# Kernel tuning notes

Hardware: AMD Instinct MI355X
Metric: run time of the kernel (lower is better)

The kernel has to match this reference:

```python
import jax, jax.numpy as jnp
import numpy as np

B, L, D = 2, 2048, 768
H = 12
HD = D // H  # 64
SCALE = HD ** -0.5


def setup_inputs() -> dict:
    key = jax.random.key(0)
    k1, k2, k3 = jax.random.split(key, 3)
    x = jax.random.normal(k1, (B, L, D), dtype=jnp.float32)
    mask = jnp.ones((B, L), dtype=jnp.int32)
    # nn.Linear weights: [out_features, in_features]
    Wqkv = jax.random.normal(k2, (3 * D, D), dtype=jnp.float32) * (D ** -0.5)
    bqkv = jnp.zeros((3 * D,), dtype=jnp.float32)
    Wout = jax.random.normal(k3, (D, D), dtype=jnp.float32) * (D ** -0.5)
    bout = jnp.zeros((D,), dtype=jnp.float32)
    return {"x": x, "mask": mask, "Wqkv": Wqkv, "bqkv": bqkv, "Wout": Wout, "bout": bout}


def reference(x, mask, Wqkv, bqkv, Wout, bout):
    Bx, Lx, Dx = x.shape
    # qkv projection: [B,L,3D] -> [3,B,H,L,HD]
    qkv = x @ Wqkv.T + bqkv
    qkv = qkv.reshape(Bx, Lx, 3, H, HD).transpose(2, 0, 3, 1, 4)
    q, k, v = qkv[0], qkv[1], qkv[2]
    # scores [B,H,L,L]
    attn = jnp.einsum('bhqd,bhkd->bhqk', q, k) * SCALE
    attn = jnp.where(mask[:, None, None, :] == 0, -jnp.inf, attn)
    attn = jax.nn.softmax(attn, axis=-1)
    # dropout p=0.0 -> identity
    out = jnp.einsum('bhqk,bhkd->bhqd', attn, v)
    out = out.transpose(0, 2, 1, 3).reshape(Bx, Lx, Dx)
    return out @ Wout.T + bout
```

## Files before the change

### kernel.cpp

```cpp
#include <hip/hip_runtime.h>
#include <hip/hip_bf16.h>

#define DEV __device__ __forceinline__

typedef __bf16 bf16_t;
typedef bf16_t bf16x8 __attribute__((ext_vector_type(8)));
typedef float f32x4 __attribute__((ext_vector_type(4)));
typedef float f32x16 __attribute__((ext_vector_type(16)));
typedef unsigned int u32x4 __attribute__((ext_vector_type(4)));

constexpr int Bc = 2, Lc = 2048, Dc = 768, Hc = 12, HDc = 64;
constexpr int NTOK = Bc * Lc;
constexpr int QKVN = 3 * Dc;
constexpr float ATT_SCALE = 0.125f;
constexpr float LOG2E = 1.44269504088896f;

DEV unsigned short f2bf(float f) {
  unsigned int u = __builtin_bit_cast(unsigned int, f);
  u += 0x7FFFu + ((u >> 16) & 1u);
  return (unsigned short)(u >> 16);
}

DEV bf16x8 ld16(const unsigned short* p) {
  return __builtin_bit_cast(bf16x8, *reinterpret_cast<const u32x4*>(p));
}

DEV unsigned cvtpk(float lo, float hi) {
  unsigned r;
  asm("v_cvt_pk_bf16_f32 %0, %1, %2" : "=v"(r) : "v"(lo), "v"(hi));
  return r;
}

DEV void gload16(const unsigned short* g, unsigned short* l) {
  __builtin_amdgcn_global_load_lds(
      (const __attribute__((address_space(1))) unsigned int*)g,
      (__attribute__((address_space(3))) unsigned int*)l, 16, 0, 0);
}

__global__ __launch_bounds__(256) void prep_kernel(
    const float* __restrict__ x, const float* __restrict__ Wqkv,
    const float* __restrict__ Wout, const int* __restrict__ mask,
    unsigned short* __restrict__ xb, unsigned short* __restrict__ wqkvb,
    unsigned short* __restrict__ woutb, float* __restrict__ mb,
    int* __restrict__ mflag) {
  const int bid = blockIdx.x, tid = threadIdx.x;
  const float* src; unsigned short* dst; int base;
  if (bid < 3072)      { src = x;    dst = xb;    base = bid; }
  else if (bid < 4800) { src = Wqkv; dst = wqkvb; base = bid - 3072; }
  else if (bid < 5376) { src = Wout; dst = woutb; base = bid - 4800; }
  else {
    int i = (bid - 5376) * 256 + tid;
    int mv = mask[i];
    mb[i] = mv ? 0.f : -1e30f;
    unsigned long long anyz = __ballot(mv == 0);
    if ((tid & 63) == 0) mflag[i >> 6] = (anyz != 0ull) ? 1 : 0;
    return;
  }
  int i = (base * 256 + tid) * 4;
  float4 v = *reinterpret_cast<const float4*>(src + i);
  ushort4 o;
  o.x = f2bf(v.x); o.y = f2bf(v.y); o.z = f2bf(v.z); o.w = f2bf(v.w);
  *reinterpret_cast<ushort4*>(dst + i) = o;
}

template <int MODE>
__global__ __launch_bounds__(256) void gemm_bt(
    const unsigned short* __restrict__ A,
    const unsigned short* __restrict__ Bw,
    const float* __restrict__ bias,
    unsigned short* __restrict__ qb, unsigned short* __restrict__ kb,
    unsigned short* __restrict__ vtb,
    float* __restrict__ Y,
    int M, int N, int K) {
  constexpr int BM = (MODE == 0) ? 128 : 64;
  constexpr int BN = 96, BK = 64;
  constexpr int AI = BM * BK / 2048;
  constexpr int MR = BM / 32;
  __shared__ alignas(16) unsigned short a_lds[BM * BK];
  __shared__ alignas(16) unsigned short b_lds[BN * BK];
  __shared__ alignas(16) unsigned short qk_patch[(MODE == 0) ? 4 : 1][16][56];

  const int tid = threadIdx.x;
  const int lane = tid & 63;
  const int l15 = lane & 15, lg = lane >> 4;
  const int wave = tid >> 6;
  const int wr = wave >> 1, wc = wave & 1;

  const int nm = M / BM;
  const int nwg = nm * (N / BN);
  const int t = (blockIdx.x & 7) * (nwg >> 3) + (blockIdx.x >> 3);
  const int m0 = (t % nm) * BM;
  const int n0 = (t / nm) * BN;

  f32x4 acc[MR][3] = {};

  for (int k0 = 0; k0 < K; k0 += BK) {
#pragma unroll
    for (int i = 0; i < AI; ++i) {
      int cc = i * 256 + tid;
      int row = cc >> 3, col = (cc & 7) * 8;
      gload16(A + (size_t)(m0 + row) * K + k0 + col, &a_lds[(i * 256 + wave * 64) * 8]);
    }
#pragma unroll
    for (int i = 0; i < 3; ++i) {
      int cc = i * 256 + tid;
      int row = cc >> 3, col = (cc & 7) * 8;
      gload16(Bw + (size_t)(n0 + row) * K + k0 + col, &b_lds[(i * 256 + wave * 64) * 8]);
    }
    __syncthreads();
#pragma unroll
    for (int kk = 0; kk < 2; ++kk) {
      bf16x8 af[MR], bfr[3];
#pragma unroll
      for (int m = 0; m < MR; ++m) {
        int row = wr * (MR * 16) + m * 16 + l15;
        af[m] = ld16(&a_lds[row * BK + kk * 32 + lg * 8]);
      }
#pragma unroll
      for (int n = 0; n < 3; ++n) {
        int row = wc * 48 + n * 16 + l15;
        bfr[n] = ld16(&b_lds[row * BK + kk * 32 + lg * 8]);
      }
#pragma unroll
      for (int m = 0; m < MR; ++m)
#pragma unroll
        for (int n = 0; n < 3; ++n)
          acc[m][n] = __builtin_amdgcn_mfma_f32_16x16x32_bf16(af[m], bfr[n], acc[m][n], 0, 0, 0);
    }
    __syncthreads();
  }

  if constexpr (MODE == 0) {
    const int base_col = n0 + wc * 48;
    const int s = n0 / Dc;
    if (s == 2) {
#pragma unroll
      for (int m = 0; m < 4; ++m) {
        int lq = m0 + wr * 64 + m * 16 + lg * 4;
        int b = lq >> 11, lql = lq & 2047;
#pragma unroll
        for (int n = 0; n < 3; ++n) {
          int cbase = base_col + n * 16;
          int h = (cbase % Dc) >> 6;
          int d = (cbase & 63) + l15;
          float bv = bias[cbase + l15];
          ushort4 o;
#pragma unroll
          for (int j = 0; j < 4; ++j)
            ((unsigned short*)&o)[j] = f2bf(acc[m][n][j] + bv);
          *reinterpret_cast<ushort4*>(
              vtb + ((size_t)(b * Hc + h) * HDc + d) * Lc + lql) = o;
        }
      }
    } else {
      unsigned short* dst = (s == 0) ? qb : kb;
      const float sc = (s == 0) ? (ATT_SCALE * LOG2E) : 1.0f;
#pragma unroll
      for (int m = 0; m < 4; ++m) {
#pragma unroll
        for (int n = 0; n < 3; ++n) {
          float bv = bias[base_col + n * 16 + l15];
#pragma unroll
          for (int j = 0; j < 4; ++j)
            qk_patch[wave][lg * 4 + j][n * 16 + l15] =
                f2bf((acc[m][n][j] + bv) * sc);
        }
#pragma unroll
        for (int i = 0; i < 2; ++i) {
          int task = i * 64 + lane;
          if (task < 96) {
            int r = task / 6, ch = task - r * 6;
            int gcol = base_col + ch * 8;
            int h = (gcol % Dc) >> 6;
            int d0 = gcol & 63;
            int lq = m0 + wr * 64 + m * 16 + r;
            int b = lq >> 11, lql = lq & 2047;
            u32x4 v = *reinterpret_cast<const u32x4*>(&qk_patch[wave][r][ch * 8]);
            *reinterpret_cast<u32x4*>(
                dst + ((size_t)(b * Hc + h) * Lc + lql) * HDc + d0) = v;
          }
        }
      }
    }
  } else {
#pragma unroll
    for (int m = 0; m < MR; ++m) {
      int row_base = m0 + wr * (MR * 16) + m * 16 + lg * 4;
#pragma unroll
      for (int n = 0; n < 3; ++n) {
        int col = n0 + wc * 48 + n * 16 + l15;
        float bv = bias[col];
#pragma unroll
        for (int j = 0; j < 4; ++j)
          Y[(size_t)(row_base + j) * Dc + col] = acc[m][n][j] + bv;
      }
    }
  }
}

__global__ __launch_bounds__(256) void attn_kernel(
    const unsigned short* __restrict__ qb,
    const unsigned short* __restrict__ kb,
    const unsigned short* __restrict__ vtb,
    const float* __restrict__ mb,
    const int* __restrict__ mflag,
    unsigned short* __restrict__ aout) {
  __shared__ alignas(16) unsigned short k_lds[4][4096];
  __shared__ alignas(16) unsigned short v_lds[2][4096];
  __shared__ float l_lds[2][32];
  const int tid = threadIdx.x;
  const int lane = tid & 63;
  const int l31 = lane & 31;
  const int hi = lane >> 5;
  const int wave = tid >> 6;
  const int ws = wave & 1;
  const int g = wave >> 1;
  const int f = blockIdx.x;
  const int loc = f >> 3;
  const int bh = (f & 7) * 3 + (loc >> 5);
  const int b = bh / Hc, h = bh % Hc;
  const int q0 = (loc & 31) * 64 + ws * 32;

  const unsigned short* Kbh = kb + (size_t)bh * Lc * HDc;
  const unsigned short* Vbh = vtb + (size_t)bh * HDc * Lc;
  const float* mbb = mb + b * Lc + hi * 4;
  const int* mfp = mflag + b * (Lc / 64);

  unsigned long long mbits;
  {
    int mv = (lane < 32) ? mfp[lane] : 0;
    mbits = __ballot(mv != 0);
  }

  bf16x8 qf[4];
  {
    const unsigned short* Qp = qb + ((size_t)bh * Lc + q0 + l31) * HDc + hi * 8;
#pragma unroll
    for (int c = 0; c < 4; ++c) qf[c] = ld16(Qp + c * 16);
  }

  bf16x8 onesf;
  {
    u32x4 ow = {0x3F803F80u, 0x3F803F80u, 0x3F803F80u, 0x3F803F80u};
    onesf = __builtin_bit_cast(bf16x8, ow);
  }

  f32x16 accO[2] = {};
  f32x16 accL = {};

  const int j0 = wave * 2, j1 = j0 + 1;
  const int r80 = j0 * 8 + (lane >> 3), r81 = r80 + 8;
  const int csw0 = (((lane & 7) ^ (lane >> 3) ^ (j0 & 3))) << 3;
  const int csw1 = (((lane & 7) ^ (lane >> 3) ^ (j1 & 3))) << 3;
  const unsigned short* kp0 = Kbh + (size_t)r80 * HDc + csw0;
  const unsigned short* kp1 = Kbh + (size_t)r81 * HDc + csw1;
  const unsigned short* vp0 = Vbh + (size_t)r80 * Lc + csw0;
  const unsigned short* vp1 = Vbh + (size_t)r81 * Lc + csw1;

#define STAGEK(buf)                               \
  {                                               \
    gload16(kp0, &k_lds[buf][j0 * 512]);          \
    gload16(kp1, &k_lds[buf][j1 * 512]);          \
    kp0 += 64 * HDc; kp1 += 64 * HDc;             \
  }
#define STAGEV(buf)                               \
  {                                               \
    gload16(vp0, &v_lds[buf][j0 * 512]);          \
    gload16(vp1, &v_lds[buf][j1 * 512]);          \
    vp0 += 64; vp1 += 64;                         \
  }

  const int swz = ((l31 & 7) ^ (l31 >> 3)) << 3;
  const int krow = (g * 32 + l31) * 64;

  STAGEK(0) STAGEK(1) STAGEV(0)
  asm volatile("s_waitcnt vmcnt(0)" ::: "memory");
  __builtin_amdgcn_s_barrier();
  f32x16 s = {};
#pragma unroll
  for (int c = 0; c < 4; ++c) {
    int ch = (((c * 2 + hi) << 3) ^ swz);
    s = __builtin_amdgcn_mfma_f32_32x32x16_bf16(
        ld16(&k_lds[0][0] + krow + ch), qf[c], s, 0, 0, 0);
  }
  STAGEK(2) STAGEV(1)

  constexpr int NSTEP = Lc / 64;
  for (int t = 0; t < NSTEP; ++t) {
    if (t + 3 < NSTEP) STAGEK((t + 3) & 3)

    f32x16 s2 = {};
    if (t + 1 < NSTEP) {
      const unsigned short* kl = &k_lds[(t + 1) & 3][0];
      __builtin_amdgcn_s_setprio(1);
#pragma unroll
      for (int c = 0; c < 4; ++c) {
        int ch = (((c * 2 + hi) << 3) ^ swz);
        s2 = __builtin_amdgcn_mfma_f32_32x32x16_bf16(
            ld16(kl + krow + ch), qf[c], s2, 0, 0, 0);
      }
      __builtin_amdgcn_s_setprio(0);
    }

    if ((mbits >> t) & 1ull) {
      const int kvt = t * 64 + g * 32;
#pragma unroll
      for (int gg = 0; gg < 4; ++gg) {
        float4 m0v = *reinterpret_cast<const float4*>(mbb + kvt + gg * 8);
        s[gg * 4 + 0] += m0v.x; s[gg * 4 + 1] += m0v.y;
        s[gg * 4 + 2] += m0v.z; s[gg * 4 + 3] += m0v.w;
      }
    }
#pragma unroll
    for (int i = 0; i < 16; ++i) s[i] = __builtin_amdgcn_exp2f(s[i]);
    bf16x8 pf[2];
#pragma unroll
    for (int c = 0; c < 2; ++c) {
      const int o = c * 8;
      unsigned pk01 = cvtpk(s[o + 0], s[o + 1]);
      unsigned pk23 = cvtpk(s[o + 2], s[o + 3]);
      unsigned pk45 = cvtpk(s[o + 4], s[o + 5]);
      unsigned pk67 = cvtpk(s[o + 6], s[o + 7]);
      asm("v_permlane32_swap_b32 %0, %1" : "+v"(pk01), "+v"(pk45));
      asm("v_permlane32_swap_b32 %0, %1" : "+v"(pk23), "+v"(pk67));
      u32x4 w = {pk01, pk23, pk45, pk67};
      pf[c] = __builtin_bit_cast(bf16x8, w);
    }
    accL = __builtin_amdgcn_mfma_f32_32x32x16_bf16(onesf, pf[0], accL, 0, 0, 0);
    accL = __builtin_amdgcn_mfma_f32_32x32x16_bf16(onesf, pf[1], accL, 0, 0, 0);
    {
      const unsigned short* vl = &v_lds[t & 1][0];
      __builtin_amdgcn_s_setprio(1);
#pragma unroll
      for (int dt = 0; dt < 2; ++dt) {
#pragma unroll
        for (int c = 0; c < 2; ++c) {
          int ch = (((g * 4 + c * 2 + hi) << 3) ^ swz);
          accO[dt] = __builtin_amdgcn_mfma_f32_32x32x16_bf16(
              ld16(vl + (dt * 32 + l31) * 64 + ch), pf[c], accO[dt], 0, 0, 0);
        }
      }
      __builtin_amdgcn_s_setprio(0);
    }
    if (t < NSTEP - 3) {
      asm volatile("s_waitcnt vmcnt(2)" ::: "memory");
    } else {
      asm volatile("s_waitcnt vmcnt(0)" ::: "memory");
    }
    __builtin_amdgcn_s_barrier();
    __builtin_amdgcn_sched_barrier(0);
    if (t + 2 < NSTEP) STAGEV((t) & 1)
    s = s2;
  }

  __syncthreads();
  const float l_run = accL[0];
  float* mO = (float*)&k_lds[0][0];
  if (g == 1) {
#pragma unroll
    for (int dt = 0; dt < 2; ++dt)
#pragma unroll
      for (int i = 0; i < 16; ++i)
        mO[(ws * 32 + dt * 16 + i) * 64 + lane] = accO[dt][i];
    if (hi == 0) l_lds[ws][l31] = l_run;
  }
  __syncthreads();
  if (g == 0) {
    float rl = 1.0f / (l_run + l_lds[ws][l31]);
    const int q = q0 + l31;
    unsigned short* op = aout + ((size_t)(b * Lc + q)) * Dc + h * HDc;
#pragma unroll
    for (int dt = 0; dt < 2; ++dt)
#pragma unroll
      for (int gg = 0; gg < 4; ++gg) {
        ushort4 o;
#pragma unroll
        for (int j = 0; j < 4; ++j) {
          int i = gg * 4 + j;
          float v = (accO[dt][i] + mO[(ws * 32 + dt * 16 + i) * 64 + lane]) * rl;
          ((unsigned short*)&o)[j] = f2bf(v);
        }
        *reinterpret_cast<ushort4*>(op + dt * 32 + gg * 8 + hi * 4) = o;
      }
  }
}

extern "C" void kernel_launch(void* const* d_in, const int* in_sizes, int n_in,
                              void* d_out, int out_size, void* d_ws, size_t ws_size,
                              hipStream_t stream) {
  const float* x    = (const float*)d_in[0];
  const int*   mask = (const int*)d_in[1];
  const float* Wqkv = (const float*)d_in[2];
  const float* bqkv = (const float*)d_in[3];
  const float* Wout = (const float*)d_in[4];
  const float* bout = (const float*)d_in[5];
  float* out = (float*)d_out;

  constexpr size_t NX   = (size_t)NTOK * Dc;
  constexpr size_t NWQ  = (size_t)QKVN * Dc;
  constexpr size_t NWO  = (size_t)Dc * Dc;
  unsigned short* w = (unsigned short*)d_ws;
  unsigned short* xb    = w;            w += NX;
  unsigned short* wqkvb = w;            w += NWQ;
  unsigned short* woutb = w;            w += NWO;
  unsigned short* qbuf  = w;            w += NX;
  unsigned short* kbuf  = w;            w += NX;
  unsigned short* vtb   = w;            w += NX;
  unsigned short* aoutb = w;            w += NX;
  float* mbf = (float*)w;               w += 2 * NTOK;
  int* mflag = (int*)w;

  prep_kernel<<<5392, 256, 0, stream>>>(x, Wqkv, Wout, mask, xb, wqkvb, woutb, mbf, mflag);

  gemm_bt<0><<<(NTOK / 128) * (QKVN / 96), 256, 0, stream>>>(
      xb, wqkvb, bqkv, qbuf, kbuf, vtb, nullptr, NTOK, QKVN, Dc);

  attn_kernel<<<dim3(768), 256, 0, stream>>>(qbuf, kbuf, vtb, mbf, mflag, aoutb);

  gemm_bt<1><<<(NTOK / 64) * (Dc / 96), 256, 0, stream>>>(
      aoutb, woutb, bout, nullptr, nullptr, nullptr, out, NTOK, Dc, Dc);
}
```

Before: 93.13 us.

## Unroll attention loop by two with ping-pong scores and stagger block starts

Rewrites the KV loop as a macro unrolled by two, alternating two score registers so the s=s2 copy disappears and the loop-edge conditions become compile-time constants in the peeled tail iterations. The QK MFMA chain now starts from a constant zero accumulator. Also adds s_sleep delays at kernel start that differ by block index modulo 3, to stagger blocks so their memory and MFMA phases overlap less in lockstep. The sleeps add a small fixed latency per block and the larger unrolled body raises code size.

```diff
diff --git a/kernel.cpp b/kernel.cpp
--- a/kernel.cpp
+++ b/kernel.cpp
@@ -221,6 +221,12 @@
   const int b = bh / Hc, h = bh % Hc;
   const int q0 = (loc & 31) * 64 + ws * 32;
 
+  {
+    const int ph = f % 3;
+    if (ph == 1) { asm volatile("s_sleep 8\n\ts_sleep 8"); }
+    else if (ph == 2) { asm volatile("s_sleep 8\n\ts_sleep 8\n\ts_sleep 8\n\ts_sleep 8"); }
+  }
+
   const unsigned short* Kbh = kb + (size_t)bh * Lc * HDc;
   const unsigned short* Vbh = vtb + (size_t)bh * HDc * Lc;
   const float* mbb = mb + b * Lc + hi * 4;
@@ -247,6 +253,7 @@
 
   f32x16 accO[2] = {};
   f32x16 accL = {};
+  const f32x16 fz = {};
 
   const int j0 = wave * 2, j1 = j0 + 1;
   const int r80 = j0 * 8 + (lane >> 3), r81 = r80 + 8;
@@ -272,86 +279,90 @@
 
   const int swz = ((l31 & 7) ^ (l31 >> 3)) << 3;
   const int krow = (g * 32 + l31) * 64;
+  const int ch0 = ((0 * 2 + hi) << 3) ^ swz;
+  const int ch1 = ((1 * 2 + hi) << 3) ^ swz;
+  const int ch2 = ((2 * 2 + hi) << 3) ^ swz;
+  const int ch3 = ((3 * 2 + hi) << 3) ^ swz;
+
+#define ITER(T, SCUR, SNEXT, DOK, DOQK, VMN, DOV)                                     \
+  {                                                                                   \
+    if (DOK) STAGEK((T + 3) & 3)                                                      \
+    if (DOQK) {                                                                       \
+      const unsigned short* kl = &k_lds[(T + 1) & 3][0];                              \
+      __builtin_amdgcn_s_setprio(1);                                                  \
+      SNEXT = __builtin_amdgcn_mfma_f32_32x32x16_bf16(ld16(kl + krow + ch0), qf[0], fz, 0, 0, 0);    \
+      SNEXT = __builtin_amdgcn_mfma_f32_32x32x16_bf16(ld16(kl + krow + ch1), qf[1], SNEXT, 0, 0, 0); \
+      SNEXT = __builtin_amdgcn_mfma_f32_32x32x16_bf16(ld16(kl + krow + ch2), qf[2], SNEXT, 0, 0, 0); \
+      SNEXT = __builtin_amdgcn_mfma_f32_32x32x16_bf16(ld16(kl + krow + ch3), qf[3], SNEXT, 0, 0, 0); \
+      __builtin_amdgcn_s_setprio(0);                                                  \
+    }                                                                                 \
+    if ((mbits >> (T)) & 1ull) {                                                      \
+      const int kvt = (T) * 64 + g * 32;                                              \
+      _Pragma("unroll")                                                               \
+      for (int gg = 0; gg < 4; ++gg) {                                                \
+        float4 m0v = *reinterpret_cast<const float4*>(mbb + kvt + gg * 8);            \
+        SCUR[gg * 4 + 0] += m0v.x; SCUR[gg * 4 + 1] += m0v.y;                         \
+        SCUR[gg * 4 + 2] += m0v.z; SCUR[gg * 4 + 3] += m0v.w;                         \
+      }                                                                               \
+    }                                                                                 \
+    _Pragma("unroll")                                                                 \
+    for (int i = 0; i < 16; ++i) SCUR[i] = __builtin_amdgcn_exp2f(SCUR[i]);           \
+    bf16x8 pf[2];                                                                     \
+    _Pragma("unroll")                                                                 \
+    for (int c = 0; c < 2; ++c) {                                                     \
+      const int o = c * 8;                                                            \
+      unsigned pk01 = cvtpk(SCUR[o + 0], SCUR[o + 1]);                                \
+      unsigned pk23 = cvtpk(SCUR[o + 2], SCUR[o + 3]);                                \
+      unsigned pk45 = cvtpk(SCUR[o + 4], SCUR[o + 5]);                                \
+      unsigned pk67 = cvtpk(SCUR[o + 6], SCUR[o + 7]);                                \
+      asm("v_permlane32_swap_b32 %0, %1" : "+v"(pk01), "+v"(pk45));                   \
+      asm("v_permlane32_swap_b32 %0, %1" : "+v"(pk23), "+v"(pk67));                   \
+      u32x4 w = {pk01, pk23, pk45, pk67};                                             \
+      pf[c] = __builtin_bit_cast(bf16x8, w);                                          \
+    }                                                                                 \
+    accL = __builtin_amdgcn_mfma_f32_32x32x16_bf16(onesf, pf[0], accL, 0, 0, 0);      \
+    accL = __builtin_amdgcn_mfma_f32_32x32x16_bf16(onesf, pf[1], accL, 0, 0, 0);      \
+    {                                                                                 \
+      const unsigned short* vl = &v_lds[(T) & 1][0];                                  \
+      __builtin_amdgcn_s_setprio(1);                                                  \
+      _Pragma("unroll")                                                               \
+      for (int dt = 0; dt < 2; ++dt) {                                                \
+        _Pragma("unroll")                                                             \
+        for (int c = 0; c < 2; ++c) {                                                 \
+          int chv = (((g * 4 + c * 2 + hi) << 3) ^ swz);                              \
+          accO[dt] = __builtin_amdgcn_mfma_f32_32x32x16_bf16(                         \
+              ld16(vl + (dt * 32 + l31) * 64 + chv), pf[c], accO[dt], 0, 0, 0);       \
+        }                                                                             \
+      }                                                                               \
+      __builtin_amdgcn_s_setprio(0);                                                  \
+    }                                                                                 \
+    asm volatile("s_waitcnt vmcnt(" #VMN ")" ::: "memory");                           \
+    __builtin_amdgcn_s_barrier();                                                     \
+    __builtin_amdgcn_sched_barrier(0);                                                \
+    if (DOV) STAGEV((T) & 1)                                                          \
+  }
 
   STAGEK(0) STAGEK(1) STAGEV(0)
   asm volatile("s_waitcnt vmcnt(0)" ::: "memory");
   __builtin_amdgcn_s_barrier();
-  f32x16 s = {};
-#pragma unroll
-  for (int c = 0; c < 4; ++c) {
-    int ch = (((c * 2 + hi) << 3) ^ swz);
-    s = __builtin_amdgcn_mfma_f32_32x32x16_bf16(
-        ld16(&k_lds[0][0] + krow + ch), qf[c], s, 0, 0, 0);
+  f32x16 sA, sB;
+  {
+    const unsigned short* kl = &k_lds[0][0];
+    sA = __builtin_amdgcn_mfma_f32_32x32x16_bf16(ld16(kl + krow + ch0), qf[0], fz, 0, 0, 0);
+    sA = __builtin_amdgcn_mfma_f32_32x32x16_bf16(ld16(kl + krow + ch1), qf[1], sA, 0, 0, 0);
+    sA = __builtin_amdgcn_mfma_f32_32x32x16_bf16(ld16(kl + krow + ch2), qf[2], sA, 0, 0, 0);
+    sA = __builtin_amdgcn_mfma_f32_32x32x16_bf16(ld16(kl + krow + ch3), qf[3], sA, 0, 0, 0);
   }
   STAGEK(2) STAGEV(1)
 
-  constexpr int NSTEP = Lc / 64;
-  for (int t = 0; t < NSTEP; ++t) {
-    if (t + 3 < NSTEP) STAGEK((t + 3) & 3)
-
-    f32x16 s2 = {};
-    if (t + 1 < NSTEP) {
-      const unsigned short* kl = &k_lds[(t + 1) & 3][0];
-      __builtin_amdgcn_s_setprio(1);
-#pragma unroll
-      for (int c = 0; c < 4; ++c) {
-        int ch = (((c * 2 + hi) << 3) ^ swz);
-        s2 = __builtin_amdgcn_mfma_f32_32x32x16_bf16(
-            ld16(kl + krow + ch), qf[c], s2, 0, 0, 0);
-      }
-      __builtin_amdgcn_s_setprio(0);
-    }
-
-    if ((mbits >> t) & 1ull) {
-      const int kvt = t * 64 + g * 32;
-#pragma unroll
-      for (int gg = 0; gg < 4; ++gg) {
-        float4 m0v = *reinterpret_cast<const float4*>(mbb + kvt + gg * 8);
-        s[gg * 4 + 0] += m0v.x; s[gg * 4 + 1] += m0v.y;
-        s[gg * 4 + 2] += m0v.z; s[gg * 4 + 3] += m0v.w;
-      }
-    }
-#pragma unroll
-    for (int i = 0; i < 16; ++i) s[i] = __builtin_amdgcn_exp2f(s[i]);
-    bf16x8 pf[2];
-#pragma unroll
-    for (int c = 0; c < 2; ++c) {
-      const int o = c * 8;
-      unsigned pk01 = cvtpk(s[o + 0], s[o + 1]);
-      unsigned pk23 = cvtpk(s[o + 2], s[o + 3]);
-      unsigned pk45 = cvtpk(s[o + 4], s[o + 5]);
-      unsigned pk67 = cvtpk(s[o + 6], s[o + 7]);
-      asm("v_permlane32_swap_b32 %0, %1" : "+v"(pk01), "+v"(pk45));
-      asm("v_permlane32_swap_b32 %0, %1" : "+v"(pk23), "+v"(pk67));
-      u32x4 w = {pk01, pk23, pk45, pk67};
-      pf[c] = __builtin_bit_cast(bf16x8, w);
-    }
-    accL = __builtin_amdgcn_mfma_f32_32x32x16_bf16(onesf, pf[0], accL, 0, 0, 0);
-    accL = __builtin_amdgcn_mfma_f32_32x32x16_bf16(onesf, pf[1], accL, 0, 0, 0);
-    {
-      const unsigned short* vl = &v_lds[t & 1][0];
-      __builtin_amdgcn_s_setprio(1);
-#pragma unroll
-      for (int dt = 0; dt < 2; ++dt) {
-#pragma unroll
-        for (int c = 0; c < 2; ++c) {
-          int ch = (((g * 4 + c * 2 + hi) << 3) ^ swz);
-          accO[dt] = __builtin_amdgcn_mfma_f32_32x32x16_bf16(
-              ld16(vl + (dt * 32 + l31) * 64 + ch), pf[c], accO[dt], 0, 0, 0);
-        }
-      }
-      __builtin_amdgcn_s_setprio(0);
-    }
-    if (t < NSTEP - 3) {
-      asm volatile("s_waitcnt vmcnt(2)" ::: "memory");
-    } else {
-      asm volatile("s_waitcnt vmcnt(0)" ::: "memory");
-    }
-    __builtin_amdgcn_s_barrier();
-    __builtin_amdgcn_sched_barrier(0);
-    if (t + 2 < NSTEP) STAGEV((t) & 1)
-    s = s2;
-  }
+  for (int t = 0; t < 28; t += 2) {
+    ITER(t,     sA, sB, true, true, 2, true)
+    ITER(t + 1, sB, sA, true, true, 2, true)
+  }
+  ITER(28, sA, sB, true,  true,  2, true)
+  ITER(29, sB, sA, false, true,  0, true)
+  ITER(30, sA, sB, false, true,  0, false)
+  ITER(31, sB, sA, false, false, 0, false)
 
   __syncthreads();
   const float l_run = accL[0];
```

Measured after the change: 107.9 us. +15.8%, slower.

## Have each attention wave process two query tiles, halving block waves

Applied to the files above, without the earlier changes.

The attention block drops from four waves to two. Each wave now handles both 32-row query tiles instead of one, so every K and V fragment read from LDS feeds two MFMAs, and each wave issues four staging loads instead of two. The aim is to cut LDS read traffic per MFMA and raise per-wave instruction-level parallelism. In exchange, register pressure roughly doubles for the accumulators and score tiles, there are fewer waves to hide latency, and the wait counts are adjusted to match.

```diff
diff --git a/kernel.cpp b/kernel.cpp
--- a/kernel.cpp
+++ b/kernel.cpp
@@ -198,7 +198,7 @@
   }
 }
 
-__global__ __launch_bounds__(256) void attn_kernel(
+__global__ __launch_bounds__(128, 2) void attn_kernel(
     const unsigned short* __restrict__ qb,
     const unsigned short* __restrict__ kb,
     const unsigned short* __restrict__ vtb,
@@ -213,13 +213,12 @@
   const int l31 = lane & 31;
   const int hi = lane >> 5;
   const int wave = tid >> 6;
-  const int ws = wave & 1;
-  const int g = wave >> 1;
+  const int g = wave;
   const int f = blockIdx.x;
   const int loc = f >> 3;
   const int bh = (f & 7) * 3 + (loc >> 5);
   const int b = bh / Hc, h = bh % Hc;
-  const int q0 = (loc & 31) * 64 + ws * 32;
+  const int q0 = (loc & 31) * 64;
 
   const unsigned short* Kbh = kb + (size_t)bh * Lc * HDc;
   const unsigned short* Vbh = vtb + (size_t)bh * HDc * Lc;
@@ -232,11 +231,12 @@
     mbits = __ballot(mv != 0);
   }
 
-  bf16x8 qf[4];
-  {
-    const unsigned short* Qp = qb + ((size_t)bh * Lc + q0 + l31) * HDc + hi * 8;
-#pragma unroll
-    for (int c = 0; c < 4; ++c) qf[c] = ld16(Qp + c * 16);
+  bf16x8 qf[2][4];
+#pragma unroll
+  for (int qt = 0; qt < 2; ++qt) {
+    const unsigned short* Qp = qb + ((size_t)bh * Lc + q0 + qt * 32 + l31) * HDc + hi * 8;
+#pragma unroll
+    for (int c = 0; c < 4; ++c) qf[qt][c] = ld16(Qp + c * 16);
   }
 
   bf16x8 onesf;
@@ -245,29 +245,35 @@
     onesf = __builtin_bit_cast(bf16x8, ow);
   }
 
-  f32x16 accO[2] = {};
-  f32x16 accL = {};
-
-  const int j0 = wave * 2, j1 = j0 + 1;
-  const int r80 = j0 * 8 + (lane >> 3), r81 = r80 + 8;
-  const int csw0 = (((lane & 7) ^ (lane >> 3) ^ (j0 & 3))) << 3;
-  const int csw1 = (((lane & 7) ^ (lane >> 3) ^ (j1 & 3))) << 3;
-  const unsigned short* kp0 = Kbh + (size_t)r80 * HDc + csw0;
-  const unsigned short* kp1 = Kbh + (size_t)r81 * HDc + csw1;
-  const unsigned short* vp0 = Vbh + (size_t)r80 * Lc + csw0;
-  const unsigned short* vp1 = Vbh + (size_t)r81 * Lc + csw1;
-
-#define STAGEK(buf)                               \
-  {                                               \
-    gload16(kp0, &k_lds[buf][j0 * 512]);          \
-    gload16(kp1, &k_lds[buf][j1 * 512]);          \
-    kp0 += 64 * HDc; kp1 += 64 * HDc;             \
-  }
-#define STAGEV(buf)                               \
-  {                                               \
-    gload16(vp0, &v_lds[buf][j0 * 512]);          \
-    gload16(vp1, &v_lds[buf][j1 * 512]);          \
-    vp0 += 64; vp1 += 64;                         \
+  f32x16 accO[2][2] = {};
+  f32x16 accL[2] = {};
+
+  const unsigned short* kp[4];
+  const unsigned short* vp[4];
+#pragma unroll
+  for (int jj = 0; jj < 4; ++jj) {
+    int j = wave * 4 + jj;
+    int r8 = j * 8 + (lane >> 3);
+    int csw = (((lane & 7) ^ (lane >> 3) ^ (j & 3))) << 3;
+    kp[jj] = Kbh + (size_t)r8 * HDc + csw;
+    vp[jj] = Vbh + (size_t)r8 * Lc + csw;
+  }
+
+#define STAGEK(buf)                                                   \
+  {                                                                   \
+    _Pragma("unroll")                                                 \
+    for (int jj = 0; jj < 4; ++jj) {                                  \
+      gload16(kp[jj], &k_lds[buf][(wave * 4 + jj) * 512]);            \
+      kp[jj] += 64 * HDc;                                             \
+    }                                                                 \
+  }
+#define STAGEV(buf)                                                   \
+  {                                                                   \
+    _Pragma("unroll")                                                 \
+    for (int jj = 0; jj < 4; ++jj) {                                  \
+      gload16(vp[jj], &v_lds[buf][(wave * 4 + jj) * 512]);            \
+      vp[jj] += 64;                                                   \
+    }                                                                 \
   }
 
   const int swz = ((l31 & 7) ^ (l31 >> 3)) << 3;
@@ -276,12 +282,13 @@
   STAGEK(0) STAGEK(1) STAGEV(0)
   asm volatile("s_waitcnt vmcnt(0)" ::: "memory");
   __builtin_amdgcn_s_barrier();
-  f32x16 s = {};
+  f32x16 s[2] = {};
 #pragma unroll
   for (int c = 0; c < 4; ++c) {
     int ch = (((c * 2 + hi) << 3) ^ swz);
-    s = __builtin_amdgcn_mfma_f32_32x32x16_bf16(
-        ld16(&k_lds[0][0] + krow + ch), qf[c], s, 0, 0, 0);
+    bf16x8 kread = ld16(&k_lds[0][0] + krow + ch);
+    s[0] = __builtin_amdgcn_mfma_f32_32x32x16_bf16(kread, qf[0][c], s[0], 0, 0, 0);
+    s[1] = __builtin_amdgcn_mfma_f32_32x32x16_bf16(kread, qf[1][c], s[1], 0, 0, 0);
   }
   STAGEK(2) STAGEV(1)
 
@@ -289,15 +296,16 @@
   for (int t = 0; t < NSTEP; ++t) {
     if (t + 3 < NSTEP) STAGEK((t + 3) & 3)
 
-    f32x16 s2 = {};
+    f32x16 s2[2] = {};
     if (t + 1 < NSTEP) {
       const unsigned short* kl = &k_lds[(t + 1) & 3][0];
       __builtin_amdgcn_s_setprio(1);
 #pragma unroll
       for (int c = 0; c < 4; ++c) {
         int ch = (((c * 2 + hi) << 3) ^ swz);
-        s2 = __builtin_amdgcn_mfma_f32_32x32x16_bf16(
-            ld16(kl + krow + ch), qf[c], s2, 0, 0, 0);
+        bf16x8 kread = ld16(kl + krow + ch);
+        s2[0] = __builtin_amdgcn_mfma_f32_32x32x16_bf16(kread, qf[0][c], s2[0], 0, 0, 0);
+        s2[1] = __builtin_amdgcn_mfma_f32_32x32x16_bf16(kread, qf[1][c], s2[1], 0, 0, 0);
       }
       __builtin_amdgcn_s_setprio(0);
     }
@@ -307,27 +315,37 @@
 #pragma unroll
       for (int gg = 0; gg < 4; ++gg) {
         float4 m0v = *reinterpret_cast<const float4*>(mbb + kvt + gg * 8);
-        s[gg * 4 + 0] += m0v.x; s[gg * 4 + 1] += m0v.y;
-        s[gg * 4 + 2] += m0v.z; s[gg * 4 + 3] += m0v.w;
-      }
-    }
-#pragma unroll
-    for (int i = 0; i < 16; ++i) s[i] = __builtin_amdgcn_exp2f(s[i]);
-    bf16x8 pf[2];
-#pragma unroll
-    for (int c = 0; c < 2; ++c) {
-      const int o = c * 8;
-      unsigned pk01 = cvtpk(s[o + 0], s[o + 1]);
-      unsigned pk23 = cvtpk(s[o + 2], s[o + 3]);
-      unsigned pk45 = cvtpk(s[o + 4], s[o + 5]);
-      unsigned pk67 = cvtpk(s[o + 6], s[o + 7]);
-      asm("v_permlane32_swap_b32 %0, %1" : "+v"(pk01), "+v"(pk45));
-      asm("v_permlane32_swap_b32 %0, %1" : "+v"(pk23), "+v"(pk67));
-      u32x4 w = {pk01, pk23, pk45, pk67};
-      pf[c] = __builtin_bit_cast(bf16x8, w);
-    }
-    accL = __builtin_amdgcn_mfma_f32_32x32x16_bf16(onesf, pf[0], accL, 0, 0, 0);
-    accL = __builtin_amdgcn_mfma_f32_32x32x16_bf16(onesf, pf[1], accL, 0, 0, 0);
+#pragma unroll
+        for (int qt = 0; qt < 2; ++qt) {
+          s[qt][gg * 4 + 0] += m0v.x; s[qt][gg * 4 + 1] += m0v.y;
+          s[qt][gg * 4 + 2] += m0v.z; s[qt][gg * 4 + 3] += m0v.w;
+        }
+      }
+    }
+#pragma unroll
+    for (int qt = 0; qt < 2; ++qt)
+#pragma unroll
+      for (int i = 0; i < 16; ++i) s[qt][i] = __builtin_amdgcn_exp2f(s[qt][i]);
+    bf16x8 pf[2][2];
+#pragma unroll
+    for (int qt = 0; qt < 2; ++qt)
+#pragma unroll
+      for (int c = 0; c < 2; ++c) {
+        const int o = c * 8;
+        unsigned pk01 = cvtpk(s[qt][o + 0], s[qt][o + 1]);
+        unsigned pk23 = cvtpk(s[qt][o + 2], s[qt][o + 3]);
+        unsigned pk45 = cvtpk(s[qt][o + 4], s[qt][o + 5]);
+        unsigned pk67 = cvtpk(s[qt][o + 6], s[qt][o + 7]);
+        asm("v_permlane32_swap_b32 %0, %1" : "+v"(pk01), "+v"(pk45));
+        asm("v_permlane32_swap_b32 %0, %1" : "+v"(pk23), "+v"(pk67));
+        u32x4 w = {pk01, pk23, pk45, pk67};
+        pf[qt][c] = __builtin_bit_cast(bf16x8, w);
+      }
+#pragma unroll
+    for (int qt = 0; qt < 2; ++qt) {
+      accL[qt] = __builtin_amdgcn_mfma_f32_32x32x16_bf16(onesf, pf[qt][0], accL[qt], 0, 0, 0);
+      accL[qt] = __builtin_amdgcn_mfma_f32_32x32x16_bf16(onesf, pf[qt][1], accL[qt], 0, 0, 0);
+    }
     {
       const unsigned short* vl = &v_lds[t & 1][0];
       __builtin_amdgcn_s_setprio(1);
@@ -335,53 +353,60 @@
       for (int dt = 0; dt < 2; ++dt) {
 #pragma unroll
         for (int c = 0; c < 2; ++c) {
-          int ch = (((g * 4 + c * 2 + hi) << 3) ^ swz);
-          accO[dt] = __builtin_amdgcn_mfma_f32_32x32x16_bf16(
-              ld16(vl + (dt * 32 + l31) * 64 + ch), pf[c], accO[dt], 0, 0, 0);
+          int chv = (((g * 4 + c * 2 + hi) << 3) ^ swz);
+          bf16x8 vread = ld16(vl + (dt * 32 + l31) * 64 + chv);
+          accO[0][dt] = __builtin_amdgcn_mfma_f32_32x32x16_bf16(vread, pf[0][c], accO[0][dt], 0, 0, 0);
+          accO[1][dt] = __builtin_amdgcn_mfma_f32_32x32x16_bf16(vread, pf[1][c], accO[1][dt], 0, 0, 0);
         }
       }
       __builtin_amdgcn_s_setprio(0);
     }
     if (t < NSTEP - 3) {
-      asm volatile("s_waitcnt vmcnt(2)" ::: "memory");
+      asm volatile("s_waitcnt vmcnt(4)" ::: "memory");
     } else {
       asm volatile("s_waitcnt vmcnt(0)" ::: "memory");
     }
     __builtin_amdgcn_s_barrier();
     __builtin_amdgcn_sched_barrier(0);
     if (t + 2 < NSTEP) STAGEV((t) & 1)
-    s = s2;
+#pragma unroll
+    for (int qt = 0; qt < 2; ++qt) s[qt] = s2[qt];
   }
 
   __syncthreads();
-  const float l_run = accL[0];
   float* mO = (float*)&k_lds[0][0];
   if (g == 1) {
 #pragma unroll
-    for (int dt = 0; dt < 2; ++dt)
-#pragma unroll
-      for (int i = 0; i < 16; ++i)
-        mO[(ws * 32 + dt * 16 + i) * 64 + lane] = accO[dt][i];
-    if (hi == 0) l_lds[ws][l31] = l_run;
+    for (int qt = 0; qt < 2; ++qt) {
+#pragma unroll
+      for (int dt = 0; dt < 2; ++dt)
+#pragma unroll
+        for (int i = 0; i < 16; ++i)
+          mO[(qt * 32 + dt * 16 + i) * 64 + lane] = accO[qt][dt][i];
+      if (hi == 0) l_lds[qt][l31] = accL[qt][0];
+    }
   }
   __syncthreads();
   if (g == 0) {
-    float rl = 1.0f / (l_run + l_lds[ws][l31]);
-    const int q = q0 + l31;
-    unsigned short* op = aout + ((size_t)(b * Lc + q)) * Dc + h * HDc;
-#pragma unroll
-    for (int dt = 0; dt < 2; ++dt)
-#pragma unroll
-      for (int gg = 0; gg < 4; ++gg) {
-        ushort4 o;
-#pragma unroll
-        for (int j = 0; j < 4; ++j) {
-          int i = gg * 4 + j;
-          float v = (accO[dt][i] + mO[(ws * 32 + dt * 16 + i) * 64 + lane]) * rl;
-          ((unsigned short*)&o)[j] = f2bf(v);
-        }
-        *reinterpret_cast<ushort4*>(op + dt * 32 + gg * 8 + hi * 4) = o;
-      }
+#pragma unroll
+    for (int qt = 0; qt < 2; ++qt) {
+      float rl = 1.0f / (accL[qt][0] + l_lds[qt][l31]);
+      const int q = q0 + qt * 32 + l31;
+      unsigned short* op = aout + ((size_t)(b * Lc + q)) * Dc + h * HDc;
+#pragma unroll
+      for (int dt = 0; dt < 2; ++dt)
+#pragma unroll
+        for (int gg = 0; gg < 4; ++gg) {
+          ushort4 o;
+#pragma unroll
+          for (int j = 0; j < 4; ++j) {
+            int i = gg * 4 + j;
+            float v = (accO[qt][dt][i] + mO[(qt * 32 + dt * 16 + i) * 64 + lane]) * rl;
+            ((unsigned short*)&o)[j] = f2bf(v);
+          }
+          *reinterpret_cast<ushort4*>(op + dt * 32 + gg * 8 + hi * 4) = o;
+        }
+    }
   }
 }
 
@@ -415,7 +440,7 @@
   gemm_bt<0><<<(NTOK / 128) * (QKVN / 96), 256, 0, stream>>>(
       xb, wqkvb, bqkv, qbuf, kbuf, vtb, nullptr, NTOK, QKVN, Dc);
 
-  attn_kernel<<<dim3(768), 256, 0, stream>>>(qbuf, kbuf, vtb, mbf, mflag, aoutb);
+  attn_kernel<<<dim3(768), 128, 0, stream>>>(qbuf, kbuf, vtb, mbf, mflag, aoutb);
 
   gemm_bt<1><<<(NTOK / 64) * (Dc / 96), 256, 0, stream>>>(
       aoutb, woutb, bout, nullptr, nullptr, nullptr, out, NTOK, Dc, Dc);
```

Measured after the change: 96.77 us. 3.9% more time.
